# Kernel tuning notes

Measured on AMD Instinct MI355X. Metric: run time of the kernel, lower is better.

## Reference

```python
import jax, jax.numpy as jnp
import numpy as np

B, N_PER, C, KG, KTOP, KNN = 8, 2048, 256, 16, 512, 32
N = B * N_PER
E = N * KG
EPS = 1e-5


def setup_inputs() -> dict:
    key = jax.random.key(0)
    ks = jax.random.split(key, 32)
    s = 0.05
    x = jax.random.normal(ks[0], (N, C), jnp.float32)
    x_origin = jax.random.normal(ks[1], (N, C), jnp.float32)
    xyz = jax.random.uniform(ks[2], (N, 3), jnp.float32)
    # graph: every node is a dst with KG incoming edges from random nodes of the SAME sample
    edge_dst = jnp.repeat(jnp.arange(N, dtype=jnp.int32), KG)
    src_local = jax.random.randint(ks[3], (E,), 0, N_PER, dtype=jnp.int32)
    edge_src = src_local + (edge_dst // N_PER) * N_PER
    # EdgeConv params (theta on x_j - x_i, phi on x_i)
    theta_w = jax.random.normal(ks[4], (C, C), jnp.float32) * s
    theta_b = jax.random.normal(ks[5], (C,), jnp.float32) * s
    phi_w = jax.random.normal(ks[6], (C, C), jnp.float32) * s
    phi_b = jax.random.normal(ks[7], (C,), jnp.float32) * s
    # region_score_mlp: Conv1d(C,64,1)-ReLU-BN(64)-Conv1d(64,32,1)-ReLU-BN(32)-Conv1d(32,1,1)
    w1 = jax.random.normal(ks[8], (64, C), jnp.float32) * s
    b1 = jax.random.normal(ks[9], (64,), jnp.float32) * s
    g1 = 1.0 + 0.1 * jax.random.normal(ks[10], (64,), jnp.float32)
    be1 = 0.1 * jax.random.normal(ks[11], (64,), jnp.float32)
    m1 = 0.1 * jax.random.normal(ks[12], (64,), jnp.float32)
    v1 = jax.random.uniform(ks[13], (64,), jnp.float32, 0.5, 1.5)
    w2 = jax.random.normal(ks[14], (32, 64), jnp.float32) * s
    b2 = jax.random.normal(ks[15], (32,), jnp.float32) * s
    g2 = 1.0 + 0.1 * jax.random.normal(ks[16], (32,), jnp.float32)
    be2 = 0.1 * jax.random.normal(ks[17], (32,), jnp.float32)
    m2 = 0.1 * jax.random.normal(ks[18], (32,), jnp.float32)
    v2 = jax.random.uniform(ks[19], (32,), jnp.float32, 0.5, 1.5)
    w3 = jax.random.normal(ks[20], (1, 32), jnp.float32) * s
    b3 = jax.random.normal(ks[21], (1,), jnp.float32) * s
    return dict(x=x, x_origin=x_origin, xyz=xyz, edge_src=edge_src, edge_dst=edge_dst,
                theta_w=theta_w, theta_b=theta_b, phi_w=phi_w, phi_b=phi_b,
                w1=w1, b1=b1, g1=g1, be1=be1, m1=m1, v1=v1,
                w2=w2, b2=b2, g2=g2, be2=be2, m2=m2, v2=v2, w3=w3, b3=b3)


def _bn(t, g, b, m, v):
    return (t - m) * jax.lax.rsqrt(v + EPS) * g + b


def _forward(x, x_origin, xyz, edge_src, edge_dst,
             theta_w, theta_b, phi_w, phi_b,
             w1, b1, g1, be1, m1, v1, w2, b2, g2, be2, m2, v2, w3, b3):
    # EdgeConv: h_i = max_{j->i}( theta(x_j - x_i) + phi(x_i) ), then residual add
    msg = ((x[edge_src] - x[edge_dst]) @ theta_w.T + theta_b
           + x[edge_dst] @ phi_w.T + phi_b)                      # [E, C]
    h = jax.ops.segment_max(msg, edge_dst, num_segments=N)       # [N, C]
    x1 = h + x                                                   # residual
    # per-node MLP (Conv1d kernel-size 1 == linear), BN in eval mode
    t = _bn(jax.nn.relu(x1 @ w1.T + b1), g1, be1, m1, v1)
    t = _bn(jax.nn.relu(t @ w2.T + b2), g2, be2, m2, v2)
    score = t @ w3.T + b3                                        # [N, 1]
    score_b = score.reshape(B, N_PER)                            # vps_score
    # per-batch top-k (cls=False path: select by raw score, descending)
    topk_vals, topk_idx = jax.lax.top_k(score_b, KTOP)           # [B, KTOP]
    perm = (topk_idx + jnp.arange(B, dtype=topk_idx.dtype)[:, None] * N_PER).reshape(-1)
    x_new = x1[perm].reshape(B, KTOP, C)
    x_copy = x_origin[perm].reshape(B, KTOP, -1)
    xyz_sel = xyz[perm].reshape(B, KTOP, 3)
    # rebuild 32-NN graph per sample on selected points (batched, no per-b python calls)
    d2 = jnp.sum((xyz_sel[:, :, None, :] - xyz_sel[:, None, :, :]) ** 2, axis=-1)  # [B,K,K]
    _, knn_idx = jax.lax.top_k(-d2, KNN)                         # [B, KTOP, 32]
    return knn_idx, x_new, x_copy, score_b, topk_vals


def reference(x, x_origin, xyz, edge_src, edge_dst,
              theta_w, theta_b, phi_w, phi_b,
              w1, b1, g1, be1, m1, v1, w2, b2, g2, be2, m2, v2, w3, b3):
    return _forward(x, x_origin, xyz, edge_src, edge_dst,
                    theta_w, theta_b, phi_w, phi_b,
                    w1, b1, g1, be1, m1, v1, w2, b2, g2, be2, m2, v2, w3, b3)
```

## Files before the change

kernel.cpp:

```cpp
#include <hip/hip_runtime.h>
#include <math.h>

constexpr int B     = 8;
constexpr int N_PER = 2048;
constexpr int C     = 256;
constexpr int KG    = 16;
constexpr int KTOP  = 512;
constexpr int KNN   = 32;
constexpr int N     = B * N_PER;
constexpr float EPS = 1e-5f;

__global__ __launch_bounds__(256) void k1_dual_gemm(
    const float* __restrict__ x, const float* __restrict__ thw,
    const float* __restrict__ phw, const float* __restrict__ thb,
    const float* __restrict__ phb, float* __restrict__ T, float* __restrict__ R)
{
    constexpr int BK = 16, ST = 68;
    __shared__ float Xs[BK * ST];
    __shared__ float Wt[BK * ST];
    __shared__ float Wp[BK * ST];
    const int tid  = threadIdx.x;
    const int row0 = blockIdx.x * 64;
    const int n0   = blockIdx.y * 64;
    const int tx = tid & 15, ty = tid >> 4;
    const int lm = tid >> 2, lq = (tid & 3) << 2;

    float aT[4][4] = {{0.f}}, aQ[4][4] = {{0.f}};

    for (int k0 = 0; k0 < C; k0 += BK) {
        float4 fx = *(const float4*)(x   + (size_t)(row0 + lm) * C + k0 + lq);
        float4 ft = *(const float4*)(thw + (size_t)(n0   + lm) * C + k0 + lq);
        float4 fp = *(const float4*)(phw + (size_t)(n0   + lm) * C + k0 + lq);
        __syncthreads();
        Xs[(lq + 0) * ST + lm] = fx.x;  Xs[(lq + 1) * ST + lm] = fx.y;
        Xs[(lq + 2) * ST + lm] = fx.z;  Xs[(lq + 3) * ST + lm] = fx.w;
        Wt[(lq + 0) * ST + lm] = ft.x;  Wt[(lq + 1) * ST + lm] = ft.y;
        Wt[(lq + 2) * ST + lm] = ft.z;  Wt[(lq + 3) * ST + lm] = ft.w;
        Wp[(lq + 0) * ST + lm] = fp.x;  Wp[(lq + 1) * ST + lm] = fp.y;
        Wp[(lq + 2) * ST + lm] = fp.z;  Wp[(lq + 3) * ST + lm] = fp.w;
        __syncthreads();
#pragma unroll
        for (int k = 0; k < BK; ++k) {
            float4 a4 = *(const float4*)&Xs[k * ST + (ty << 2)];
            float4 t4 = *(const float4*)&Wt[k * ST + (tx << 2)];
            float4 p4 = *(const float4*)&Wp[k * ST + (tx << 2)];
            float av[4] = {a4.x, a4.y, a4.z, a4.w};
            float tv[4] = {t4.x, t4.y, t4.z, t4.w};
            float pv[4] = {p4.x, p4.y, p4.z, p4.w};
#pragma unroll
            for (int i2 = 0; i2 < 4; ++i2)
#pragma unroll
                for (int j2 = 0; j2 < 4; ++j2) {
                    aT[i2][j2] += av[i2] * tv[j2];
                    aQ[i2][j2] += av[i2] * pv[j2];
                }
        }
    }
#pragma unroll
    for (int i2 = 0; i2 < 4; ++i2) {
        const int gm = row0 + (ty << 2) + i2;
#pragma unroll
        for (int j2 = 0; j2 < 4; ++j2) {
            const int gn = n0 + (tx << 2) + j2;
            const size_t off = (size_t)gm * C + gn;
            const float tval = aT[i2][j2];
            T[off] = tval;
            R[off] = x[off] + aQ[i2][j2] + thb[gn] + phb[gn] - tval;
        }
    }
}

__global__ __launch_bounds__(256) void k2a_gather_max(
    const int* __restrict__ esrc, const float* __restrict__ T, float* x1r)
{
    const int i = blockIdx.x;
    const int c = threadIdx.x;
    __shared__ int s[KG];
    if (c < KG) s[c] = esrc[i * KG + c];
    __syncthreads();
    float m = -INFINITY;
#pragma unroll
    for (int k = 0; k < KG; ++k) m = fmaxf(m, T[(size_t)s[k] * C + c]);
    const size_t off = (size_t)i * C + c;
    x1r[off] = m + x1r[off];
}

__global__ __launch_bounds__(256) void k2b_layer1(
    const float* __restrict__ x1, const float* __restrict__ w1,
    const float* __restrict__ b1, const float* __restrict__ g1,
    const float* __restrict__ be1, const float* __restrict__ m1,
    const float* __restrict__ v1, float* __restrict__ t1)
{
    constexpr int BK = 16, ST = 68;
    __shared__ float Xs[BK * ST];
    __shared__ float Ws[BK * ST];
    const int tid  = threadIdx.x;
    const int row0 = blockIdx.x * 64;
    const int tx = tid & 15, ty = tid >> 4;
    const int lm = tid >> 2, lq = (tid & 3) << 2;

    float acc[4][4] = {{0.f}};
    for (int k0 = 0; k0 < C; k0 += BK) {
        float4 fx = *(const float4*)(x1 + (size_t)(row0 + lm) * C + k0 + lq);
        float4 fw = *(const float4*)(w1 + (size_t)lm * C + k0 + lq);
        __syncthreads();
        Xs[(lq + 0) * ST + lm] = fx.x;  Xs[(lq + 1) * ST + lm] = fx.y;
        Xs[(lq + 2) * ST + lm] = fx.z;  Xs[(lq + 3) * ST + lm] = fx.w;
        Ws[(lq + 0) * ST + lm] = fw.x;  Ws[(lq + 1) * ST + lm] = fw.y;
        Ws[(lq + 2) * ST + lm] = fw.z;  Ws[(lq + 3) * ST + lm] = fw.w;
        __syncthreads();
#pragma unroll
        for (int k = 0; k < BK; ++k) {
            float4 a4 = *(const float4*)&Xs[k * ST + (ty << 2)];
            float4 w4 = *(const float4*)&Ws[k * ST + (tx << 2)];
            float av[4] = {a4.x, a4.y, a4.z, a4.w};
            float wv[4] = {w4.x, w4.y, w4.z, w4.w};
#pragma unroll
            for (int i2 = 0; i2 < 4; ++i2)
#pragma unroll
                for (int j2 = 0; j2 < 4; ++j2) acc[i2][j2] += av[i2] * wv[j2];
        }
    }
#pragma unroll
    for (int i2 = 0; i2 < 4; ++i2) {
        const int gm = row0 + (ty << 2) + i2;
#pragma unroll
        for (int j2 = 0; j2 < 4; ++j2) {
            const int gn = (tx << 2) + j2;
            float y = acc[i2][j2] + b1[gn];
            y = fmaxf(y, 0.f);
            const float inv = 1.0f / sqrtf(v1[gn] + EPS);
            y = (y - m1[gn]) * inv * g1[gn] + be1[gn];
            t1[(size_t)gm * 64 + gn] = y;
        }
    }
}

__global__ __launch_bounds__(256) void k2c_score(
    const float* __restrict__ t1,
    const float* __restrict__ w2, const float* __restrict__ b2,
    const float* __restrict__ g2, const float* __restrict__ be2,
    const float* __restrict__ m2, const float* __restrict__ v2,
    const float* __restrict__ w3, const float* __restrict__ b3,
    float* __restrict__ score_ws, float* __restrict__ out_score)
{
    __shared__ float w2s[32 * 65];
    __shared__ float t1s[8 * 65];
    __shared__ float zs[8 * 33];
    __shared__ float w3s[32];
    const int t = threadIdx.x;
    const int node0 = blockIdx.x * 8;

    for (int idx = t; idx < 2048; idx += 256) {
        const int oo = idx >> 6, jj = idx & 63;
        w2s[oo * 65 + jj] = w2[idx];
    }
    if (t < 32) w3s[t] = w3[t];
    for (int idx = t; idx < 512; idx += 256) {
        const int nn = idx >> 6, jj = idx & 63;
        t1s[nn * 65 + jj] = t1[(size_t)(node0 + nn) * 64 + jj];
    }
    __syncthreads();

    const int nl = t >> 5, o = t & 31;
    float z = 0.f;
#pragma unroll
    for (int j = 0; j < 64; ++j) z += t1s[nl * 65 + j] * w2s[o * 65 + j];
    z += b2[o];
    z = fmaxf(z, 0.f);
    const float inv = 1.0f / sqrtf(v2[o] + EPS);
    z = (z - m2[o]) * inv * g2[o] + be2[o];
    zs[nl * 33 + o] = z;
    __syncthreads();

    if (t < 8) {
        float s = 0.f;
#pragma unroll
        for (int j = 0; j < 32; ++j) s += zs[t * 33 + j] * w3s[j];
        s += b3[0];
        const int node = node0 + t;
        score_ws[node]  = s;
        out_score[node] = s;
    }
}

__global__ __launch_bounds__(1024) void k3_topk(
    const float* __restrict__ score, float* __restrict__ out_topk,
    int* __restrict__ perm)
{
    __shared__ unsigned long long keys[N_PER];
    const int b = blockIdx.x;
    const int t = threadIdx.x;
    for (int i = t; i < N_PER; i += 1024) {
        const float v = score[b * N_PER + i];
        unsigned u = __float_as_uint(v);
        const unsigned ua = (u & 0x80000000u) ? ~u : (u | 0x80000000u);
        const unsigned ud = ~ua;
        keys[i] = ((unsigned long long)ud << 32) | (unsigned)i;
    }
    __syncthreads();
    for (int k = 2; k <= N_PER; k <<= 1) {
        for (int j = k >> 1; j > 0; j >>= 1) {
            for (int i = t; i < N_PER; i += 1024) {
                const int ixj = i ^ j;
                if (ixj > i) {
                    const unsigned long long a = keys[i], c = keys[ixj];
                    const bool up = ((i & k) == 0);
                    if ((a > c) == up) { keys[i] = c; keys[ixj] = a; }
                }
            }
            __syncthreads();
        }
    }
    for (int r = t; r < KTOP; r += 1024) {
        const int idx = (int)(keys[r] & 0xffffffffu);
        out_topk[b * KTOP + r] = score[b * N_PER + idx];
        perm[b * KTOP + r] = b * N_PER + idx;
    }
}

__global__ __launch_bounds__(256) void k4_gather(
    const int* __restrict__ perm, const float* __restrict__ x1,
    const float* __restrict__ xorig, const float* __restrict__ xyz,
    float* __restrict__ out_xnew, float* __restrict__ out_xcopy,
    float* __restrict__ xyz_sel)
{
    const int row = blockIdx.x;
    const int t = threadIdx.x;
    const int g = perm[row];
    out_xnew [(size_t)row * C + t] = x1   [(size_t)g * C + t];
    out_xcopy[(size_t)row * C + t] = xorig[(size_t)g * C + t];
    if (t < 3) xyz_sel[row * 3 + t] = xyz[g * 3 + t];
}

__global__ __launch_bounds__(256) void k5_knn(
    const float* __restrict__ xyz_sel, float* __restrict__ out_knn)
{
    constexpr int G = 4;
    __shared__ float px[KTOP], py[KTOP], pz[KTOP];
    __shared__ unsigned long long keys[G * KTOP];
    const int t    = threadIdx.x;
    const int q0   = blockIdx.x * G;
    const int b    = q0 >> 9;
    const int i0   = q0 & 511;

    for (int idx = t; idx < KTOP; idx += 256) {
        const float* p = xyz_sel + ((size_t)b * KTOP + idx) * 3;
        px[idx] = p[0]; py[idx] = p[1]; pz[idx] = p[2];
    }
    __syncthreads();

    for (int w = t; w < G * KTOP; w += 256) {
        const int p = w >> 9, idx = w & 511;
        const float qx = px[i0 + p], qy = py[i0 + p], qz = pz[i0 + p];
        const float dx = __fsub_rn(qx, px[idx]);
        const float dy = __fsub_rn(qy, py[idx]);
        const float dz = __fsub_rn(qz, pz[idx]);
        const float d2 = __fadd_rn(__fadd_rn(__fmul_rn(dx, dx), __fmul_rn(dy, dy)),
                                   __fmul_rn(dz, dz));
        keys[w] = ((unsigned long long)__float_as_uint(d2) << 32) | (unsigned)idx;
    }
    __syncthreads();

    for (int k = 2; k <= 32; k <<= 1) {
        for (int j = k >> 1; j > 0; j >>= 1) {
            for (int i = t; i < G * KTOP; i += 256) {
                const int ixj = i ^ j;
                if (ixj > i) {
                    const int il = i & 31;
                    const unsigned long long a = keys[i], c = keys[ixj];
                    const bool up = ((il & k) == 0) || (k == 32);
                    if ((a > c) == up) { keys[i] = c; keys[ixj] = a; }
                }
            }
            __syncthreads();
        }
    }

    for (int r = 0; r < 4; ++r) {
        const int npairs = 8 >> r;
        const int total  = G * npairs * 32;
        for (int w = t; w < total; w += 256) {
            const int p  = w / (npairs * 32);
            const int rm = w - p * (npairs * 32);
            const int m  = rm >> 5, i = rm & 31;
            const int baseA = p * KTOP + m * (64 << r);
            const int baseB = baseA + (32 << r);
            const unsigned long long a = keys[baseA + i];
            const unsigned long long c = keys[baseB + 31 - i];
            keys[baseA + i] = (c < a) ? c : a;
        }
        __syncthreads();
        for (int j = 16; j > 0; j >>= 1) {
            for (int w = t; w < total; w += 256) {
                const int p  = w / (npairs * 32);
                const int rm = w - p * (npairs * 32);
                const int m  = rm >> 5, i = rm & 31;
                const int ixj = i ^ j;
                if (ixj > i) {
                    const int baseA = p * KTOP + m * (64 << r);
                    const unsigned long long a = keys[baseA + i], c = keys[baseA + ixj];
                    if (a > c) { keys[baseA + i] = c; keys[baseA + ixj] = a; }
                }
            }
            __syncthreads();
        }
    }

    if (t < G * KNN) {
        const int p = t >> 5, r = t & 31;
        out_knn[((size_t)(q0 + p)) * KNN + r] =
            (float)(unsigned)(keys[p * KTOP + r] & 0xffffffffu);
    }
}

extern "C" void kernel_launch(void* const* d_in, const int* in_sizes, int n_in,
                              void* d_out, int out_size, void* d_ws, size_t ws_size,
                              hipStream_t stream)
{
    const float* x     = (const float*)d_in[0];
    const float* xorig = (const float*)d_in[1];
    const float* xyz   = (const float*)d_in[2];
    const int*   esrc  = (const int*)d_in[3];
    const float* thw = (const float*)d_in[5];
    const float* thb = (const float*)d_in[6];
    const float* phw = (const float*)d_in[7];
    const float* phb = (const float*)d_in[8];
    const float* w1  = (const float*)d_in[9];
    const float* b1  = (const float*)d_in[10];
    const float* g1  = (const float*)d_in[11];
    const float* be1 = (const float*)d_in[12];
    const float* m1  = (const float*)d_in[13];
    const float* v1  = (const float*)d_in[14];
    const float* w2  = (const float*)d_in[15];
    const float* b2  = (const float*)d_in[16];
    const float* g2  = (const float*)d_in[17];
    const float* be2 = (const float*)d_in[18];
    const float* m2  = (const float*)d_in[19];
    const float* v2  = (const float*)d_in[20];
    const float* w3  = (const float*)d_in[21];
    const float* b3  = (const float*)d_in[22];

    float* ws   = (float*)d_ws;
    float* T    = ws;
    float* x1   = ws + (size_t)N * C;
    float* t1   = ws + 2 * (size_t)N * C;
    float* sc   = t1 + (size_t)N * 64;
    int*   perm = (int*)(sc + N);
    float* xsel = (float*)(perm + B * KTOP);

    float* out     = (float*)d_out;
    float* o_knn   = out;
    float* o_xnew  = o_knn + (size_t)B * KTOP * KNN;
    float* o_xcopy = o_xnew + (size_t)B * KTOP * C;
    float* o_score = o_xcopy + (size_t)B * KTOP * C;
    float* o_topk  = o_score + (size_t)B * N_PER;

    k1_dual_gemm<<<dim3(N / 64, C / 64), 256, 0, stream>>>(x, thw, phw, thb, phb, T, x1);
    k2a_gather_max<<<N, 256, 0, stream>>>(esrc, T, x1);
    k2b_layer1<<<dim3(N / 64, 1), 256, 0, stream>>>(x1, w1, b1, g1, be1, m1, v1, t1);
    k2c_score<<<N / 8, 256, 0, stream>>>(t1, w2, b2, g2, be2, m2, v2, w3, b3, sc, o_score);
    k3_topk<<<B, 1024, 0, stream>>>(sc, o_topk, perm);
    k4_gather<<<B * KTOP, 256, 0, stream>>>(perm, x1, xorig, xyz, o_xnew, o_xcopy, xsel);
    k5_knn<<<B * KTOP / 4, 256, 0, stream>>>(xsel, o_knn);
}
```

Baseline: 276.5 us.

## Retile dual GEMM with prefetch, vectorize gather, fuse score MLP and gather into kNN

The dual GEMM now uses 128-row tiles with 8x4 per-thread accumulators. It prefetches the next k-slice into registers and writes its epilogue with float4 stores. The edge max-gather processes four nodes per block with float4 loads. The two score-MLP kernels are fused so the hidden activations stay in shared memory, and the row/xyz gather kernel is folded into the kNN kernel. Together these cut kernel launches, global round-trips and per-thread overhead, at the cost of more registers and shared memory per block, which may lower occupancy.

Result: no change. 276.9 us (+0.1%).

```diff
diff --git a/kernel.cpp b/kernel.cpp
--- a/kernel.cpp
+++ b/kernel.cpp
@@ -10,45 +10,58 @@
 constexpr int N     = B * N_PER;
 constexpr float EPS = 1e-5f;
 
-__global__ __launch_bounds__(256) void k1_dual_gemm(
+__global__ __launch_bounds__(256, 2) void k1_dual_gemm(
     const float* __restrict__ x, const float* __restrict__ thw,
     const float* __restrict__ phw, const float* __restrict__ thb,
     const float* __restrict__ phb, float* __restrict__ T, float* __restrict__ R)
 {
-    constexpr int BK = 16, ST = 68;
-    __shared__ float Xs[BK * ST];
-    __shared__ float Wt[BK * ST];
-    __shared__ float Wp[BK * ST];
+    constexpr int BK = 16, STX = 132, STW = 68;
+    __shared__ float Xs[BK * STX];
+    __shared__ float Wt[BK * STW];
+    __shared__ float Wp[BK * STW];
     const int tid  = threadIdx.x;
-    const int row0 = blockIdx.x * 64;
+    const int row0 = blockIdx.x * 128;
     const int n0   = blockIdx.y * 64;
     const int tx = tid & 15, ty = tid >> 4;
-    const int lm = tid >> 2, lq = (tid & 3) << 2;
-
-    float aT[4][4] = {{0.f}}, aQ[4][4] = {{0.f}};
+    const int lm = tid >> 1, lq = (tid & 1) * 8;
+    const int wm = tid >> 2, wq = (tid & 3) * 4;
+
+    float aT[8][4] = {{0.f}}, aQ[8][4] = {{0.f}};
+
+    float4 nx0 = *(const float4*)(x   + (size_t)(row0 + lm) * C + lq);
+    float4 nx1 = *(const float4*)(x   + (size_t)(row0 + lm) * C + lq + 4);
+    float4 nt  = *(const float4*)(thw + (size_t)(n0   + wm) * C + wq);
+    float4 np_ = *(const float4*)(phw + (size_t)(n0   + wm) * C + wq);
 
     for (int k0 = 0; k0 < C; k0 += BK) {
-        float4 fx = *(const float4*)(x   + (size_t)(row0 + lm) * C + k0 + lq);
-        float4 ft = *(const float4*)(thw + (size_t)(n0   + lm) * C + k0 + lq);
-        float4 fp = *(const float4*)(phw + (size_t)(n0   + lm) * C + k0 + lq);
-        __syncthreads();
-        Xs[(lq + 0) * ST + lm] = fx.x;  Xs[(lq + 1) * ST + lm] = fx.y;
-        Xs[(lq + 2) * ST + lm] = fx.z;  Xs[(lq + 3) * ST + lm] = fx.w;
-        Wt[(lq + 0) * ST + lm] = ft.x;  Wt[(lq + 1) * ST + lm] = ft.y;
-        Wt[(lq + 2) * ST + lm] = ft.z;  Wt[(lq + 3) * ST + lm] = ft.w;
-        Wp[(lq + 0) * ST + lm] = fp.x;  Wp[(lq + 1) * ST + lm] = fp.y;
-        Wp[(lq + 2) * ST + lm] = fp.z;  Wp[(lq + 3) * ST + lm] = fp.w;
-        __syncthreads();
+        __syncthreads();
+        Xs[(lq + 0) * STX + lm] = nx0.x;  Xs[(lq + 1) * STX + lm] = nx0.y;
+        Xs[(lq + 2) * STX + lm] = nx0.z;  Xs[(lq + 3) * STX + lm] = nx0.w;
+        Xs[(lq + 4) * STX + lm] = nx1.x;  Xs[(lq + 5) * STX + lm] = nx1.y;
+        Xs[(lq + 6) * STX + lm] = nx1.z;  Xs[(lq + 7) * STX + lm] = nx1.w;
+        Wt[(wq + 0) * STW + wm] = nt.x;   Wt[(wq + 1) * STW + wm] = nt.y;
+        Wt[(wq + 2) * STW + wm] = nt.z;   Wt[(wq + 3) * STW + wm] = nt.w;
+        Wp[(wq + 0) * STW + wm] = np_.x;  Wp[(wq + 1) * STW + wm] = np_.y;
+        Wp[(wq + 2) * STW + wm] = np_.z;  Wp[(wq + 3) * STW + wm] = np_.w;
+        __syncthreads();
+        const int kn = k0 + BK;
+        if (kn < C) {
+            nx0 = *(const float4*)(x   + (size_t)(row0 + lm) * C + kn + lq);
+            nx1 = *(const float4*)(x   + (size_t)(row0 + lm) * C + kn + lq + 4);
+            nt  = *(const float4*)(thw + (size_t)(n0   + wm) * C + kn + wq);
+            np_ = *(const float4*)(phw + (size_t)(n0   + wm) * C + kn + wq);
+        }
 #pragma unroll
         for (int k = 0; k < BK; ++k) {
-            float4 a4 = *(const float4*)&Xs[k * ST + (ty << 2)];
-            float4 t4 = *(const float4*)&Wt[k * ST + (tx << 2)];
-            float4 p4 = *(const float4*)&Wp[k * ST + (tx << 2)];
-            float av[4] = {a4.x, a4.y, a4.z, a4.w};
-            float tv[4] = {t4.x, t4.y, t4.z, t4.w};
-            float pv[4] = {p4.x, p4.y, p4.z, p4.w};
-#pragma unroll
-            for (int i2 = 0; i2 < 4; ++i2)
+            float4 alo = *(const float4*)&Xs[k * STX + ty * 8];
+            float4 ahi = *(const float4*)&Xs[k * STX + ty * 8 + 4];
+            float4 tv4 = *(const float4*)&Wt[k * STW + tx * 4];
+            float4 pv4 = *(const float4*)&Wp[k * STW + tx * 4];
+            float av[8] = {alo.x, alo.y, alo.z, alo.w, ahi.x, ahi.y, ahi.z, ahi.w};
+            float tv[4] = {tv4.x, tv4.y, tv4.z, tv4.w};
+            float pv[4] = {pv4.x, pv4.y, pv4.z, pv4.w};
+#pragma unroll
+            for (int i2 = 0; i2 < 8; ++i2)
 #pragma unroll
                 for (int j2 = 0; j2 < 4; ++j2) {
                     aT[i2][j2] += av[i2] * tv[j2];
@@ -56,44 +69,67 @@
                 }
         }
     }
-#pragma unroll
-    for (int i2 = 0; i2 < 4; ++i2) {
-        const int gm = row0 + (ty << 2) + i2;
-#pragma unroll
-        for (int j2 = 0; j2 < 4; ++j2) {
-            const int gn = n0 + (tx << 2) + j2;
-            const size_t off = (size_t)gm * C + gn;
-            const float tval = aT[i2][j2];
-            T[off] = tval;
-            R[off] = x[off] + aQ[i2][j2] + thb[gn] + phb[gn] - tval;
-        }
+
+    const int gn = n0 + tx * 4;
+    const float4 tb4 = *(const float4*)(thb + gn);
+    const float4 pb4 = *(const float4*)(phb + gn);
+#pragma unroll
+    for (int i2 = 0; i2 < 8; ++i2) {
+        const int gm = row0 + ty * 8 + i2;
+        const size_t off = (size_t)gm * C + gn;
+        float4 xr = *(const float4*)(x + off);
+        float4 tvv = make_float4(aT[i2][0], aT[i2][1], aT[i2][2], aT[i2][3]);
+        float4 rv;
+        rv.x = xr.x + aQ[i2][0] + tb4.x + pb4.x - tvv.x;
+        rv.y = xr.y + aQ[i2][1] + tb4.y + pb4.y - tvv.y;
+        rv.z = xr.z + aQ[i2][2] + tb4.z + pb4.z - tvv.z;
+        rv.w = xr.w + aQ[i2][3] + tb4.w + pb4.w - tvv.w;
+        *(float4*)(T + off) = tvv;
+        *(float4*)(R + off) = rv;
     }
 }
 
 __global__ __launch_bounds__(256) void k2a_gather_max(
     const int* __restrict__ esrc, const float* __restrict__ T, float* x1r)
 {
-    const int i = blockIdx.x;
-    const int c = threadIdx.x;
-    __shared__ int s[KG];
-    if (c < KG) s[c] = esrc[i * KG + c];
-    __syncthreads();
-    float m = -INFINITY;
-#pragma unroll
-    for (int k = 0; k < KG; ++k) m = fmaxf(m, T[(size_t)s[k] * C + c]);
-    const size_t off = (size_t)i * C + c;
-    x1r[off] = m + x1r[off];
-}
-
-__global__ __launch_bounds__(256) void k2b_layer1(
+    const int node0 = blockIdx.x * 4;
+    const int t = threadIdx.x;
+    __shared__ int s[4][KG];
+    if (t < 64) s[t >> 4][t & 15] = esrc[(node0 + (t >> 4)) * KG + (t & 15)];
+    __syncthreads();
+    const int m  = t >> 6;
+    const int c4 = (t & 63) * 4;
+    float4 acc = make_float4(-INFINITY, -INFINITY, -INFINITY, -INFINITY);
+#pragma unroll
+    for (int k = 0; k < KG; ++k) {
+        const float4 v = *(const float4*)&T[(size_t)s[m][k] * C + c4];
+        acc.x = fmaxf(acc.x, v.x);  acc.y = fmaxf(acc.y, v.y);
+        acc.z = fmaxf(acc.z, v.z);  acc.w = fmaxf(acc.w, v.w);
+    }
+    const size_t off = (size_t)(node0 + m) * C + c4;
+    float4 r = *(const float4*)&x1r[off];
+    r.x += acc.x;  r.y += acc.y;  r.z += acc.z;  r.w += acc.w;
+    *(float4*)&x1r[off] = r;
+}
+
+__global__ __launch_bounds__(256) void k2bc_score(
     const float* __restrict__ x1, const float* __restrict__ w1,
     const float* __restrict__ b1, const float* __restrict__ g1,
     const float* __restrict__ be1, const float* __restrict__ m1,
-    const float* __restrict__ v1, float* __restrict__ t1)
+    const float* __restrict__ v1,
+    const float* __restrict__ w2, const float* __restrict__ b2,
+    const float* __restrict__ g2, const float* __restrict__ be2,
+    const float* __restrict__ m2, const float* __restrict__ v2,
+    const float* __restrict__ w3, const float* __restrict__ b3,
+    float* __restrict__ score_ws, float* __restrict__ out_score)
 {
     constexpr int BK = 16, ST = 68;
     __shared__ float Xs[BK * ST];
     __shared__ float Ws[BK * ST];
+    __shared__ float t1s[64 * 65];
+    __shared__ float w2s[32 * 65];
+    __shared__ float w3s[32];
+    __shared__ float zs[64 * 33];
     const int tid  = threadIdx.x;
     const int row0 = blockIdx.x * 64;
     const int tx = tid & 15, ty = tid >> 4;
@@ -121,66 +157,47 @@
                 for (int j2 = 0; j2 < 4; ++j2) acc[i2][j2] += av[i2] * wv[j2];
         }
     }
+    __syncthreads();
 #pragma unroll
     for (int i2 = 0; i2 < 4; ++i2) {
-        const int gm = row0 + (ty << 2) + i2;
+        const int mrow = (ty << 2) + i2;
 #pragma unroll
         for (int j2 = 0; j2 < 4; ++j2) {
-            const int gn = (tx << 2) + j2;
-            float y = acc[i2][j2] + b1[gn];
+            const int o = (tx << 2) + j2;
+            float y = acc[i2][j2] + b1[o];
             y = fmaxf(y, 0.f);
-            const float inv = 1.0f / sqrtf(v1[gn] + EPS);
-            y = (y - m1[gn]) * inv * g1[gn] + be1[gn];
-            t1[(size_t)gm * 64 + gn] = y;
-        }
-    }
-}
-
-__global__ __launch_bounds__(256) void k2c_score(
-    const float* __restrict__ t1,
-    const float* __restrict__ w2, const float* __restrict__ b2,
-    const float* __restrict__ g2, const float* __restrict__ be2,
-    const float* __restrict__ m2, const float* __restrict__ v2,
-    const float* __restrict__ w3, const float* __restrict__ b3,
-    float* __restrict__ score_ws, float* __restrict__ out_score)
-{
-    __shared__ float w2s[32 * 65];
-    __shared__ float t1s[8 * 65];
-    __shared__ float zs[8 * 33];
-    __shared__ float w3s[32];
-    const int t = threadIdx.x;
-    const int node0 = blockIdx.x * 8;
-
-    for (int idx = t; idx < 2048; idx += 256) {
-        const int oo = idx >> 6, jj = idx & 63;
-        w2s[oo * 65 + jj] = w2[idx];
-    }
-    if (t < 32) w3s[t] = w3[t];
-    for (int idx = t; idx < 512; idx += 256) {
-        const int nn = idx >> 6, jj = idx & 63;
-        t1s[nn * 65 + jj] = t1[(size_t)(node0 + nn) * 64 + jj];
-    }
-    __syncthreads();
-
-    const int nl = t >> 5, o = t & 31;
-    float z = 0.f;
-#pragma unroll
-    for (int j = 0; j < 64; ++j) z += t1s[nl * 65 + j] * w2s[o * 65 + j];
-    z += b2[o];
-    z = fmaxf(z, 0.f);
-    const float inv = 1.0f / sqrtf(v2[o] + EPS);
-    z = (z - m2[o]) * inv * g2[o] + be2[o];
-    zs[nl * 33 + o] = z;
-    __syncthreads();
-
-    if (t < 8) {
-        float s = 0.f;
-#pragma unroll
-        for (int j = 0; j < 32; ++j) s += zs[t * 33 + j] * w3s[j];
-        s += b3[0];
-        const int node = node0 + t;
-        score_ws[node]  = s;
-        out_score[node] = s;
+            y = (y - m1[o]) * (1.0f / sqrtf(v1[o] + EPS)) * g1[o] + be1[o];
+            t1s[mrow * 65 + o] = y;
+        }
+    }
+    for (int idx = tid; idx < 2048; idx += 256)
+        w2s[(idx >> 6) * 65 + (idx & 63)] = w2[idx];
+    if (tid < 32) w3s[tid] = w3[tid];
+    __syncthreads();
+
+    const int o = tid & 31;
+    const float inv2 = (1.0f / sqrtf(v2[o] + EPS)) * g2[o];
+#pragma unroll
+    for (int p = 0; p < 8; ++p) {
+        const int nl = p * 8 + (tid >> 5);
+        float z = 0.f;
+#pragma unroll
+        for (int j = 0; j < 64; ++j) z += t1s[nl * 65 + j] * w2s[o * 65 + j];
+        z += b2[o];
+        z = fmaxf(z, 0.f);
+        z = (z - m2[o]) * inv2 + be2[o];
+        zs[nl * 33 + o] = z;
+    }
+    __syncthreads();
+
+    if (tid < 64) {
+        float sacc = 0.f;
+#pragma unroll
+        for (int j = 0; j < 32; ++j) sacc += zs[tid * 33 + j] * w3s[j];
+        sacc += b3[0];
+        const int node = row0 + tid;
+        score_ws[node]  = sacc;
+        out_score[node] = sacc;
     }
 }
 
@@ -219,43 +236,40 @@
     }
 }
 
-__global__ __launch_bounds__(256) void k4_gather(
-    const int* __restrict__ perm, const float* __restrict__ x1,
-    const float* __restrict__ xorig, const float* __restrict__ xyz,
+__global__ __launch_bounds__(256) void k5_knn(
+    const int* __restrict__ perm, const float* __restrict__ xyz,
+    const float* __restrict__ x1, const float* __restrict__ xorig,
     float* __restrict__ out_xnew, float* __restrict__ out_xcopy,
-    float* __restrict__ xyz_sel)
-{
-    const int row = blockIdx.x;
-    const int t = threadIdx.x;
-    const int g = perm[row];
-    out_xnew [(size_t)row * C + t] = x1   [(size_t)g * C + t];
-    out_xcopy[(size_t)row * C + t] = xorig[(size_t)g * C + t];
-    if (t < 3) xyz_sel[row * 3 + t] = xyz[g * 3 + t];
-}
-
-__global__ __launch_bounds__(256) void k5_knn(
-    const float* __restrict__ xyz_sel, float* __restrict__ out_knn)
+    float* __restrict__ out_knn)
 {
     constexpr int G = 4;
     __shared__ float px[KTOP], py[KTOP], pz[KTOP];
     __shared__ unsigned long long keys[G * KTOP];
-    const int t    = threadIdx.x;
-    const int q0   = blockIdx.x * G;
-    const int b    = q0 >> 9;
-    const int i0   = q0 & 511;
+    const int t  = threadIdx.x;
+    const int q0 = blockIdx.x * G;
+    const int b  = q0 >> 9;
+    const int i0 = q0 & 511;
 
     for (int idx = t; idx < KTOP; idx += 256) {
-        const float* p = xyz_sel + ((size_t)b * KTOP + idx) * 3;
-        px[idx] = p[0]; py[idx] = p[1]; pz[idx] = p[2];
+        const int g = perm[b * KTOP + idx];
+        px[idx] = xyz[g * 3 + 0];
+        py[idx] = xyz[g * 3 + 1];
+        pz[idx] = xyz[g * 3 + 2];
+    }
+#pragma unroll
+    for (int p = 0; p < G; ++p) {
+        const int row = q0 + p;
+        const int g = perm[row];
+        out_xnew [(size_t)row * C + t] = x1   [(size_t)g * C + t];
+        out_xcopy[(size_t)row * C + t] = xorig[(size_t)g * C + t];
     }
     __syncthreads();
 
     for (int w = t; w < G * KTOP; w += 256) {
         const int p = w >> 9, idx = w & 511;
-        const float qx = px[i0 + p], qy = py[i0 + p], qz = pz[i0 + p];
-        const float dx = __fsub_rn(qx, px[idx]);
-        const float dy = __fsub_rn(qy, py[idx]);
-        const float dz = __fsub_rn(qz, pz[idx]);
+        const float dx = __fsub_rn(px[i0 + p], px[idx]);
+        const float dy = __fsub_rn(py[i0 + p], py[idx]);
+        const float dz = __fsub_rn(pz[i0 + p], pz[idx]);
         const float d2 = __fadd_rn(__fadd_rn(__fmul_rn(dx, dx), __fmul_rn(dy, dy)),
                                    __fmul_rn(dz, dz));
         keys[w] = ((unsigned long long)__float_as_uint(d2) << 32) | (unsigned)idx;
@@ -276,7 +290,6 @@
             __syncthreads();
         }
     }
-
     for (int r = 0; r < 4; ++r) {
         const int npairs = 8 >> r;
         const int total  = G * npairs * 32;
@@ -344,10 +357,8 @@
     float* ws   = (float*)d_ws;
     float* T    = ws;
     float* x1   = ws + (size_t)N * C;
-    float* t1   = ws + 2 * (size_t)N * C;
-    float* sc   = t1 + (size_t)N * 64;
+    float* sc   = ws + 2 * (size_t)N * C;
     int*   perm = (int*)(sc + N);
-    float* xsel = (float*)(perm + B * KTOP);
 
     float* out     = (float*)d_out;
     float* o_knn   = out;
@@ -356,11 +367,11 @@
     float* o_score = o_xcopy + (size_t)B * KTOP * C;
     float* o_topk  = o_score + (size_t)B * N_PER;
 
-    k1_dual_gemm<<<dim3(N / 64, C / 64), 256, 0, stream>>>(x, thw, phw, thb, phb, T, x1);
-    k2a_gather_max<<<N, 256, 0, stream>>>(esrc, T, x1);
-    k2b_layer1<<<dim3(N / 64, 1), 256, 0, stream>>>(x1, w1, b1, g1, be1, m1, v1, t1);
-    k2c_score<<<N / 8, 256, 0, stream>>>(t1, w2, b2, g2, be2, m2, v2, w3, b3, sc, o_score);
+    k1_dual_gemm<<<dim3(N / 128, C / 64), 256, 0, stream>>>(x, thw, phw, thb, phb, T, x1);
+    k2a_gather_max<<<N / 4, 256, 0, stream>>>(esrc, T, x1);
+    k2bc_score<<<N / 64, 256, 0, stream>>>(x1, w1, b1, g1, be1, m1, v1,
+                                           w2, b2, g2, be2, m2, v2, w3, b3, sc, o_score);
     k3_topk<<<B, 1024, 0, stream>>>(sc, o_topk, perm);
-    k4_gather<<<B * KTOP, 256, 0, stream>>>(perm, x1, xorig, xyz, o_xnew, o_xcopy, xsel);
-    k5_knn<<<B * KTOP / 4, 256, 0, stream>>>(xsel, o_knn);
-}
+    k5_knn<<<B * KTOP / 4, 256, 0, stream>>>(perm, xyz, x1, xorig,
+                                             o_xnew, o_xcopy, o_knn);
+}
```
